# Kernel optimization log

Hardware: AMD Instinct MI355X
Metric: run time of the kernel (lower is better)

Reference implementation:

```python
import jax, jax.numpy as jnp
import numpy as np
from jax.scipy.special import ndtri

N = 2097152
SQRT2 = 1.4142135623730951
TWO_PI = 6.283185307179586

# 32-point Gauss-Legendre nodes/weights mapped to [0, 1]
_gx, _gw = np.polynomial.legendre.leggauss(32)
_GL_X = jnp.asarray(0.5 * (_gx + 1.0), dtype=jnp.float32)  # [Q]
_GL_W = jnp.asarray(0.5 * _gw, dtype=jnp.float32)          # [Q]


def _phi(x):
    # standard normal CDF
    return 0.5 * (1.0 + jax.lax.erf(x / SQRT2))


def _bvn_cdf(h, k, rho):
    """P(X<=h, Y<=k) for standard bivariate normal with correlation rho.
    Genz identity: Phi2 = Phi(h)Phi(k) + rho/(2pi) * int_0^1 f(rho*t) dt.
    h, k: [N]; rho: scalar."""
    r = rho * _GL_X                     # [Q]
    omr2 = 1.0 - r * r                  # [Q]
    hh = h[:, None]
    kk = k[:, None]
    integrand = jnp.exp(-(hh * hh + kk * kk - 2.0 * r * hh * kk) / (2.0 * omr2)) / jnp.sqrt(omr2)  # [N,Q]
    return _phi(h) * _phi(k) + (rho / TWO_PI) * (integrand @ _GL_W)


def setup_inputs() -> dict:
    key = jax.random.key(0)
    k1, k2, k3, k4, k5 = jax.random.split(key, 5)
    # probabilities for binary outcomes, strictly inside (0,1)
    p3 = jax.random.uniform(k1, (N,), jnp.float32, 0.02, 0.98)
    p4 = jax.random.uniform(k2, (N,), jnp.float32, 0.02, 0.98)
    cont_hat = jax.random.normal(k3, (2, N), jnp.float32)
    y_hat = jnp.stack([p3, cont_hat[0], p4, cont_hat[1]], axis=0)  # [4,N]
    lab = (jax.random.uniform(k4, (2, N), jnp.float32) < 0.5).astype(jnp.float32)
    cont_y = cont_hat + 0.5 * jax.random.normal(k5, (2, N), jnp.float32)
    y = jnp.stack([lab[0], cont_y[0], lab[1], cont_y[1]], axis=0)  # [4,N]
    gamma12 = jnp.array([[1.0, 0.3], [0.3, 1.0]], jnp.float32)
    gamma34 = jnp.array([[1.0, 0.2], [0.2, 1.0]], jnp.float32)
    gamma3412 = jnp.array([[0.4, 0.1], [0.05, 0.3]], jnp.float32)
    sigma1 = jnp.ones((1,), jnp.float32)
    sigma2 = jnp.ones((1,), jnp.float32)
    return {"y_hat": y_hat, "y": y, "gamma12": gamma12, "gamma34": gamma34,
            "gamma3412": gamma3412, "sigma1": sigma1, "sigma2": sigma2}


def reference(y_hat, y, gamma12, gamma34, gamma3412, sigma1, sigma2):
    gamma12_inv = jnp.linalg.inv(gamma12)                         # [2,2]
    V_tilde = gamma34 - gamma3412 @ gamma12_inv @ gamma3412.T     # [2,2]

    y3 = y[0, :]
    y4 = y[2, :]
    p3 = y_hat[0, :]
    p4 = y_hat[2, :]

    ei = y - y_hat
    st_e1 = ei[1, :] / sigma1
    st_e2 = ei[3, :] / sigma2
    q12 = jnp.stack([st_e1, st_e2], axis=0)                       # [2,N]

    mu_tilde = gamma3412 @ (gamma12_inv @ q12)                    # [2,N]
    mu1, mu2 = mu_tilde[0], mu_tilde[1]
    V11, V22, V12 = V_tilde[0, 0], V_tilde[1, 1], V_tilde[0, 1]
    s1 = jnp.sqrt(V11)
    s2 = jnp.sqrt(V22)
    rho = V12 / (s1 * s2)

    a1 = -ndtri(p3)
    a2 = -ndtri(p4)

    h = (a1 - mu1) / s1
    k = (a2 - mu2) / s2
    phi2 = _bvn_cdf(h, k, rho)

    C = ((1.0 - 2.0 * y3) * (1.0 - 2.0 * y4) * phi2
         + y3 * (1.0 - 2.0 * y4) * _phi(k)
         + y4 * (1.0 - 2.0 * y3) * _phi(h)
         + y3 * y4)
    logC = jnp.log(C)

    # quadratic form q12^T gamma12_inv q12 / 2 per sample
    quad = 0.5 * jnp.einsum("in,ij,jn->n", q12, gamma12_inv, q12)
    loss = jnp.sum(quad - logC)
    return loss
```

## Files before the change

kernel.cpp:

```cpp
#include <hip/hip_runtime.h>
#include <math.h>

#define N_ELEM 2097152
#define SQRT2F     1.41421356237309504880f
#define INV_SQRT2F 0.70710678118654752440f
#define INV_TWO_PI 0.15915494309189533577f
#define LOG2E      1.44269504088896340736f
#define LN2        0.69314718055994530942f
#define NBLOCKS    2048

__device__ __constant__ float GL8_T[8] = {
    0.01985507175123185f, 0.10166676129318664f, 0.23723379504183550f,
    0.40828267875217511f, 0.59171732124782489f, 0.76276620495816450f,
    0.89833323870681336f, 0.98014492824876815f };
__device__ __constant__ float GL8_W[8] = {
    0.05061426814518815f, 0.11119051722668725f, 0.15685332293894365f,
    0.18134189168918100f, 0.18134189168918100f, 0.15685332293894365f,
    0.11119051722668725f, 0.05061426814518815f };

__device__ __forceinline__ float erfinv_fast(float x) {
    float w = -LN2 * __builtin_amdgcn_logf(fmaf(-x, x, 1.0f));
    w -= 2.5f;
    float p = 2.81022636e-08f;
    p = fmaf(p, w, 3.43273939e-07f);
    p = fmaf(p, w, -3.5233877e-06f);
    p = fmaf(p, w, -4.39150654e-06f);
    p = fmaf(p, w, 0.00021858087f);
    p = fmaf(p, w, -0.00125372503f);
    p = fmaf(p, w, -0.00417768164f);
    p = fmaf(p, w, 0.246640727f);
    p = fmaf(p, w, 1.50140941f);
    return p * x;
}

__device__ __forceinline__ float phi_fast(float h, float hh) {
    float az = fabsf(h) * INV_SQRT2F;
    float t  = __builtin_amdgcn_rcpf(fmaf(0.3275911f, az, 1.0f));
    float P  = 1.061405429f;
    P = fmaf(P, t, -1.453152027f);
    P = fmaf(P, t,  1.421413741f);
    P = fmaf(P, t, -0.284496736f);
    P = fmaf(P, t,  0.254829592f);
    P = P * t;
    float E = __builtin_amdgcn_exp2f(hh * (-0.5f * LOG2E));
    float half_pe = 0.5f * P * E;
    return (h >= 0.0f) ? (1.0f - half_pe) : half_pe;
}

__global__ __launch_bounds__(256) void parametric_loss_stage1(
    const float* __restrict__ y_hat, const float* __restrict__ y,
    const float* __restrict__ g12,   const float* __restrict__ g34,
    const float* __restrict__ g3412, const float* __restrict__ sig1,
    const float* __restrict__ sig2,  float* __restrict__ partials)
{
    __shared__ float wave_sums[4];

    float G00 = g12[0], G01 = g12[1], G10 = g12[2], G11 = g12[3];
    float invdet = 1.0f / (G00 * G11 - G01 * G10);
    float I00 =  G11 * invdet, I01 = -G01 * invdet;
    float I10 = -G10 * invdet, I11 =  G00 * invdet;
    float P00 = g3412[0], P01 = g3412[1], P10 = g3412[2], P11 = g3412[3];
    float A00 = P00 * I00 + P01 * I10;
    float A01 = P00 * I01 + P01 * I11;
    float A10 = P10 * I00 + P11 * I10;
    float A11 = P10 * I01 + P11 * I11;
    float V00 = g34[0] - (A00 * P00 + A01 * P01);
    float V01 = g34[1] - (A00 * P10 + A01 * P11);
    float V22 = g34[3] - (A10 * P10 + A11 * P11);
    float s1 = sqrtf(V00), s2 = sqrtf(V22);
    float rho = V01 / (s1 * s2);
    float inv_s1 = 1.0f / s1, inv_s2 = 1.0f / s2;
    float isig1 = 1.0f / sig1[0], isig2 = 1.0f / sig2[0];
    float rho_2pi = rho * INV_TWO_PI;

    float c1L[8], c2L[8], cwv[8];
    #pragma unroll
    for (int i = 0; i < 8; ++i) {
        float r = rho * GL8_T[i];
        float omr2 = 1.0f - r * r;
        float io = 1.0f / omr2;
        c1L[i] = 0.5f * io * LOG2E;
        c2L[i] = r * io * LOG2E;
        cwv[i] = GL8_W[i] * rsqrtf(omr2);
    }

    int tid  = blockIdx.x * 256 + threadIdx.x;
    int base = tid * 4;

    float4 p3v  = *(const float4*)(y_hat + 0 * N_ELEM + base);
    float4 ch1  = *(const float4*)(y_hat + 1 * N_ELEM + base);
    float4 p4v  = *(const float4*)(y_hat + 2 * N_ELEM + base);
    float4 ch2  = *(const float4*)(y_hat + 3 * N_ELEM + base);
    float4 y3v  = *(const float4*)(y     + 0 * N_ELEM + base);
    float4 cy1  = *(const float4*)(y     + 1 * N_ELEM + base);
    float4 y4v  = *(const float4*)(y     + 2 * N_ELEM + base);
    float4 cy2  = *(const float4*)(y     + 3 * N_ELEM + base);

    const float* p3a = (const float*)&p3v;  const float* ch1a = (const float*)&ch1;
    const float* p4a = (const float*)&p4v;  const float* ch2a = (const float*)&ch2;
    const float* y3a = (const float*)&y3v;  const float* cy1a = (const float*)&cy1;
    const float* y4a = (const float*)&y4v;  const float* cy2a = (const float*)&cy2;

    float hhkk[4], hk1[4], integ[4], Ph[4], Pk[4], quadv[4];

    #pragma unroll
    for (int j = 0; j < 4; ++j) {
        float q1 = (cy1a[j] - ch1a[j]) * isig1;
        float q2 = (cy2a[j] - ch2a[j]) * isig2;
        float mu1 = A00 * q1 + A01 * q2;
        float mu2 = A10 * q1 + A11 * q2;
        quadv[j] = 0.5f * (q1 * (I00 * q1 + I01 * q2) + q2 * (I10 * q1 + I11 * q2));
        float a1 = -SQRT2F * erfinv_fast(fmaf(2.0f, p3a[j], -1.0f));
        float a2 = -SQRT2F * erfinv_fast(fmaf(2.0f, p4a[j], -1.0f));
        float h = (a1 - mu1) * inv_s1;
        float k = (a2 - mu2) * inv_s2;
        float hh = h * h, kk = k * k;
        Ph[j] = phi_fast(h, hh);
        Pk[j] = phi_fast(k, kk);
        hhkk[j] = hh + kk;
        hk1[j]  = h * k;
        integ[j] = 0.0f;
    }

    #pragma unroll
    for (int i = 0; i < 8; ++i) {
        float c1 = c1L[i], c2 = c2L[i], cw = cwv[i];
        #pragma unroll
        for (int j = 0; j < 4; ++j) {
            float e = __builtin_amdgcn_exp2f(fmaf(hk1[j], c2, -hhkk[j] * c1));
            integ[j] = fmaf(cw, e, integ[j]);
        }
    }

    float acc = 0.0f;
    #pragma unroll
    for (int j = 0; j < 4; ++j) {
        float phi2 = fmaf(rho_2pi, integ[j], Ph[j] * Pk[j]);
        float y3 = y3a[j], y4 = y4a[j];
        float om3 = fmaf(-2.0f, y3, 1.0f), om4 = fmaf(-2.0f, y4, 1.0f);
        float C = om3 * om4 * phi2 + y3 * om4 * Pk[j] + y4 * om3 * Ph[j] + y3 * y4;
        acc += quadv[j] - LN2 * __builtin_amdgcn_logf(C);
    }

    #pragma unroll
    for (int off = 32; off > 0; off >>= 1)
        acc += __shfl_down(acc, off, 64);
    int lane = threadIdx.x & 63, wid = threadIdx.x >> 6;
    if (lane == 0) wave_sums[wid] = acc;
    __syncthreads();
    if (threadIdx.x == 0) {
        partials[blockIdx.x] = wave_sums[0] + wave_sums[1] + wave_sums[2] + wave_sums[3];
    }
}

__global__ __launch_bounds__(256) void parametric_loss_stage2(
    const float* __restrict__ partials, float* __restrict__ out)
{
    __shared__ float wave_sums[4];
    int t = threadIdx.x;
    float4 a = *(const float4*)(partials + t * 8);
    float4 b = *(const float4*)(partials + t * 8 + 4);
    float acc = (a.x + a.y) + (a.z + a.w) + (b.x + b.y) + (b.z + b.w);
    #pragma unroll
    for (int off = 32; off > 0; off >>= 1)
        acc += __shfl_down(acc, off, 64);
    int lane = t & 63, wid = t >> 6;
    if (lane == 0) wave_sums[wid] = acc;
    __syncthreads();
    if (t == 0)
        out[0] = wave_sums[0] + wave_sums[1] + wave_sums[2] + wave_sums[3];
}

extern "C" void kernel_launch(void* const* d_in, const int* in_sizes, int n_in,
                              void* d_out, int out_size, void* d_ws, size_t ws_size,
                              hipStream_t stream) {
    const float* y_hat = (const float*)d_in[0];
    const float* y     = (const float*)d_in[1];
    const float* g12   = (const float*)d_in[2];
    const float* g34   = (const float*)d_in[3];
    const float* g3412 = (const float*)d_in[4];
    const float* sig1  = (const float*)d_in[5];
    const float* sig2  = (const float*)d_in[6];
    float* out      = (float*)d_out;
    float* partials = (float*)d_ws;

    parametric_loss_stage1<<<NBLOCKS, 256, 0, stream>>>(
        y_hat, y, g12, g34, g3412, sig1, sig2, partials);
    parametric_loss_stage2<<<1, 256, 0, stream>>>(partials, out);
}
```

Before: 107.9 us.

## Use persistent grid-stride blocks with register double-buffered prefetch of inputs

Shrinks the grid from 2048 to 512 blocks, each thread now handling four chunks of four elements in a grid-stride loop. The next chunk's eight float4 loads are issued into a second register buffer before the current chunk is computed, so memory latency overlaps with the transcendental-heavy math. The per-block setup of constants is amortised over more work, and stage 2 is resized to read 512 partials. The cost is extra register pressure from the double buffer, which may reduce occupancy; launch bounds now request two blocks per CU.

```diff
diff --git a/kernel.cpp b/kernel.cpp
--- a/kernel.cpp
+++ b/kernel.cpp
@@ -7,7 +7,11 @@
 #define INV_TWO_PI 0.15915494309189533577f
 #define LOG2E      1.44269504088896340736f
 #define LN2        0.69314718055994530942f
-#define NBLOCKS    2048
+
+#define TPB      256
+#define NBLOCKS  512
+#define NTHREADS (TPB * NBLOCKS)
+#define ITERS    4
 
 __device__ __constant__ float GL8_T[8] = {
     0.01985507175123185f, 0.10166676129318664f, 0.23723379504183550f,
@@ -47,7 +51,7 @@
     return (h >= 0.0f) ? (1.0f - half_pe) : half_pe;
 }
 
-__global__ __launch_bounds__(256) void parametric_loss_stage1(
+__global__ __launch_bounds__(TPB, 2) void parametric_loss_stage1(
     const float* __restrict__ y_hat, const float* __restrict__ y,
     const float* __restrict__ g12,   const float* __restrict__ g34,
     const float* __restrict__ g3412, const float* __restrict__ sig1,
@@ -72,6 +76,8 @@
     float inv_s1 = 1.0f / s1, inv_s2 = 1.0f / s2;
     float isig1 = 1.0f / sig1[0], isig2 = 1.0f / sig2[0];
     float rho_2pi = rho * INV_TWO_PI;
+    float ce1 = -SQRT2F * inv_s1;
+    float ce2 = -SQRT2F * inv_s2;
 
     float c1L[8], c2L[8], cwv[8];
     #pragma unroll
@@ -84,62 +90,81 @@
         cwv[i] = GL8_W[i] * rsqrtf(omr2);
     }
 
-    int tid  = blockIdx.x * 256 + threadIdx.x;
-    int base = tid * 4;
-
-    float4 p3v  = *(const float4*)(y_hat + 0 * N_ELEM + base);
-    float4 ch1  = *(const float4*)(y_hat + 1 * N_ELEM + base);
-    float4 p4v  = *(const float4*)(y_hat + 2 * N_ELEM + base);
-    float4 ch2  = *(const float4*)(y_hat + 3 * N_ELEM + base);
-    float4 y3v  = *(const float4*)(y     + 0 * N_ELEM + base);
-    float4 cy1  = *(const float4*)(y     + 1 * N_ELEM + base);
-    float4 y4v  = *(const float4*)(y     + 2 * N_ELEM + base);
-    float4 cy2  = *(const float4*)(y     + 3 * N_ELEM + base);
-
-    const float* p3a = (const float*)&p3v;  const float* ch1a = (const float*)&ch1;
-    const float* p4a = (const float*)&p4v;  const float* ch2a = (const float*)&ch2;
-    const float* y3a = (const float*)&y3v;  const float* cy1a = (const float*)&cy1;
-    const float* y4a = (const float*)&y4v;  const float* cy2a = (const float*)&cy2;
-
-    float hhkk[4], hk1[4], integ[4], Ph[4], Pk[4], quadv[4];
-
-    #pragma unroll
-    for (int j = 0; j < 4; ++j) {
-        float q1 = (cy1a[j] - ch1a[j]) * isig1;
-        float q2 = (cy2a[j] - ch2a[j]) * isig2;
-        float mu1 = A00 * q1 + A01 * q2;
-        float mu2 = A10 * q1 + A11 * q2;
-        quadv[j] = 0.5f * (q1 * (I00 * q1 + I01 * q2) + q2 * (I10 * q1 + I11 * q2));
-        float a1 = -SQRT2F * erfinv_fast(fmaf(2.0f, p3a[j], -1.0f));
-        float a2 = -SQRT2F * erfinv_fast(fmaf(2.0f, p4a[j], -1.0f));
-        float h = (a1 - mu1) * inv_s1;
-        float k = (a2 - mu2) * inv_s2;
-        float hh = h * h, kk = k * k;
-        Ph[j] = phi_fast(h, hh);
-        Pk[j] = phi_fast(k, kk);
-        hhkk[j] = hh + kk;
-        hk1[j]  = h * k;
-        integ[j] = 0.0f;
-    }
-
-    #pragma unroll
-    for (int i = 0; i < 8; ++i) {
-        float c1 = c1L[i], c2 = c2L[i], cw = cwv[i];
+    const int tid = blockIdx.x * TPB + threadIdx.x;
+
+    float4 cur[8], nxt[8];
+
+    {
+        int base = tid * 4;
+        #pragma unroll
+        for (int r = 0; r < 4; ++r) {
+            cur[r]     = *(const float4*)(y_hat + r * N_ELEM + base);
+            cur[r + 4] = *(const float4*)(y     + r * N_ELEM + base);
+        }
+    }
+
+    float acc = 0.0f;
+
+    #pragma unroll
+    for (int it = 0; it < ITERS; ++it) {
+        if (it + 1 < ITERS) {
+            int base = ((it + 1) * NTHREADS + tid) * 4;
+            #pragma unroll
+            for (int r = 0; r < 4; ++r) {
+                nxt[r]     = *(const float4*)(y_hat + r * N_ELEM + base);
+                nxt[r + 4] = *(const float4*)(y     + r * N_ELEM + base);
+            }
+        }
+
+        const float* p3a  = (const float*)&cur[0];
+        const float* ch1a = (const float*)&cur[1];
+        const float* p4a  = (const float*)&cur[2];
+        const float* ch2a = (const float*)&cur[3];
+        const float* y3a  = (const float*)&cur[4];
+        const float* cy1a = (const float*)&cur[5];
+        const float* y4a  = (const float*)&cur[6];
+        const float* cy2a = (const float*)&cur[7];
+
+        float hhkk[4], hk1[4], integ[4], Ph[4], Pk[4];
+
         #pragma unroll
         for (int j = 0; j < 4; ++j) {
-            float e = __builtin_amdgcn_exp2f(fmaf(hk1[j], c2, -hhkk[j] * c1));
-            integ[j] = fmaf(cw, e, integ[j]);
-        }
-    }
-
-    float acc = 0.0f;
-    #pragma unroll
-    for (int j = 0; j < 4; ++j) {
-        float phi2 = fmaf(rho_2pi, integ[j], Ph[j] * Pk[j]);
-        float y3 = y3a[j], y4 = y4a[j];
-        float om3 = fmaf(-2.0f, y3, 1.0f), om4 = fmaf(-2.0f, y4, 1.0f);
-        float C = om3 * om4 * phi2 + y3 * om4 * Pk[j] + y4 * om3 * Ph[j] + y3 * y4;
-        acc += quadv[j] - LN2 * __builtin_amdgcn_logf(C);
+            float q1 = (cy1a[j] - ch1a[j]) * isig1;
+            float q2 = (cy2a[j] - ch2a[j]) * isig2;
+            float mu1 = A00 * q1 + A01 * q2;
+            float mu2 = A10 * q1 + A11 * q2;
+            acc += 0.5f * (q1 * (I00 * q1 + I01 * q2) + q2 * (I10 * q1 + I11 * q2));
+            float h = fmaf(ce1, erfinv_fast(fmaf(2.0f, p3a[j], -1.0f)), -mu1 * inv_s1);
+            float k = fmaf(ce2, erfinv_fast(fmaf(2.0f, p4a[j], -1.0f)), -mu2 * inv_s2);
+            float hh = h * h, kk = k * k;
+            Ph[j] = phi_fast(h, hh);
+            Pk[j] = phi_fast(k, kk);
+            hhkk[j] = hh + kk;
+            hk1[j]  = h * k;
+            integ[j] = 0.0f;
+        }
+
+        #pragma unroll
+        for (int i = 0; i < 8; ++i) {
+            float c1 = c1L[i], c2 = c2L[i], cw = cwv[i];
+            #pragma unroll
+            for (int j = 0; j < 4; ++j) {
+                float e = __builtin_amdgcn_exp2f(fmaf(hk1[j], c2, -hhkk[j] * c1));
+                integ[j] = fmaf(cw, e, integ[j]);
+            }
+        }
+
+        #pragma unroll
+        for (int j = 0; j < 4; ++j) {
+            float phi2 = fmaf(rho_2pi, integ[j], Ph[j] * Pk[j]);
+            float y3 = y3a[j], y4 = y4a[j];
+            float om3 = fmaf(-2.0f, y3, 1.0f), om4 = fmaf(-2.0f, y4, 1.0f);
+            float C = om3 * om4 * phi2 + y3 * om4 * Pk[j] + y4 * om3 * Ph[j] + y3 * y4;
+            acc -= LN2 * __builtin_amdgcn_logf(C);
+        }
+
+        #pragma unroll
+        for (int r = 0; r < 8; ++r) cur[r] = nxt[r];
     }
 
     #pragma unroll
@@ -158,9 +183,8 @@
 {
     __shared__ float wave_sums[4];
     int t = threadIdx.x;
-    float4 a = *(const float4*)(partials + t * 8);
-    float4 b = *(const float4*)(partials + t * 8 + 4);
-    float acc = (a.x + a.y) + (a.z + a.w) + (b.x + b.y) + (b.z + b.w);
+    float2 a = *(const float2*)(partials + t * 2);
+    float acc = a.x + a.y;
     #pragma unroll
     for (int off = 32; off > 0; off >>= 1)
         acc += __shfl_down(acc, off, 64);
@@ -184,7 +208,7 @@
     float* out      = (float*)d_out;
     float* partials = (float*)d_ws;
 
-    parametric_loss_stage1<<<NBLOCKS, 256, 0, stream>>>(
+    parametric_loss_stage1<<<NBLOCKS, TPB, 0, stream>>>(
         y_hat, y, g12, g34, g3412, sig1, sig2, partials);
     parametric_loss_stage2<<<1, 256, 0, stream>>>(partials, out);
 }
```

New measurement: 106.0 us. Within noise of the previous version (-1.8%).
